# Kernel tuning notes

Measured on AMD Instinct MI355X. Metric: run time of the kernel, lower is better.

The kernel has to match this reference:

```python
import jax, jax.numpy as jnp
import numpy as np
from jax import lax

N, D_IN, D_H, D_A, N_CLS, K = 50000, 1024, 512, 256, 2, 8


def setup_inputs() -> dict:
    key = jax.random.key(0)
    ks = jax.random.split(key, 13)
    s = 0.02
    return {
        "h": jax.random.normal(ks[0], (1, N, D_IN), dtype=jnp.float32),
        "fc_W": jax.random.normal(ks[1], (D_H, D_IN), dtype=jnp.float32) * s,
        "fc_b": jnp.zeros((D_H,), jnp.float32),
        "att_a_W": jax.random.normal(ks[2], (D_A, D_H), dtype=jnp.float32) * s,
        "att_a_b": jnp.zeros((D_A,), jnp.float32),
        "att_b_W": jax.random.normal(ks[3], (D_A, D_H), dtype=jnp.float32) * s,
        "att_b_b": jnp.zeros((D_A,), jnp.float32),
        "att_c_W": jax.random.normal(ks[4], (1, D_A), dtype=jnp.float32) * s,
        "att_c_b": jnp.zeros((1,), jnp.float32),
        "cls_W": jax.random.normal(ks[5], (N_CLS, D_H), dtype=jnp.float32) * s,
        "cls_b": jnp.zeros((N_CLS,), jnp.float32),
        "inst_W": jax.random.normal(ks[6], (2, D_H), dtype=jnp.float32) * s,
        "inst_b": jnp.zeros((2,), jnp.float32),
        "label": 1,  # one_hot -> [0,1]: inst_eval runs only for classifier index 1
    }


def reference(h, fc_W, fc_b, att_a_W, att_a_b, att_b_W, att_b_b,
              att_c_W, att_c_b, cls_W, cls_b, inst_W, inst_b, label):
    x = jnp.squeeze(h, 0)                               # [N, 1024]
    hh = jax.nn.relu(x @ fc_W.T + fc_b)                 # [N, 512]
    # gated attention: tanh gate * sigmoid gate -> scalar score per instance
    a = jnp.tanh(hh @ att_a_W.T + att_a_b)              # [N, 256]
    b = jax.nn.sigmoid(hh @ att_b_W.T + att_b_b)        # [N, 256]
    A_raw = (a * b) @ att_c_W.T + att_c_b               # [N, 1]
    A = jax.nn.softmax(A_raw, axis=0)                   # softmax over instances

    # instance eval (label==1, subtyping=False -> only classifier index 1)
    scores = A_raw[:, 0]                                # [N]
    _, top_p_ids = lax.top_k(scores, K)
    _, top_n_ids = lax.top_k(-scores, K)
    ids = jnp.concatenate([top_p_ids, top_n_ids])       # [2K]
    inst = hh[ids]                                      # gather [2K, 512]
    logits = inst @ inst_W.T + inst_b                   # [2K, 2]
    targets = jnp.concatenate([jnp.ones((K,), jnp.int32),
                               jnp.zeros((K,), jnp.int32)])
    logp = jax.nn.log_softmax(logits, axis=-1)
    instance_loss = -jnp.mean(jnp.take_along_axis(logp, targets[:, None], axis=1))

    instance_scores = hh @ cls_W.T + cls_b              # [N, 2]
    preds = (instance_scores * A).sum(axis=0) / A.sum(axis=0)  # [2]
    preds = preds[None, :]                              # [1, 2]
    return preds, instance_scores, A_raw, instance_loss
```

## Files before the change

kernel.cpp:

```cpp
#include <hip/hip_runtime.h>
#include <hip/hip_bf16.h>
#include <math.h>

typedef __bf16 bf16_t;
typedef __bf16 bf16x8 __attribute__((ext_vector_type(8)));
typedef float  f32x4  __attribute__((ext_vector_type(4)));

#define NROWS 50000

typedef const __attribute__((address_space(1))) unsigned int* gp_t;
typedef __attribute__((address_space(3))) unsigned int* lp_t;
__device__ __forceinline__ void cp16(void* l, const void* g) {
    __builtin_amdgcn_global_load_lds((gp_t)g, (lp_t)l, 16, 0, 0);
}

__global__ void k_convert(const float* __restrict__ fcW,
                          const float* __restrict__ aW,
                          const float* __restrict__ bW,
                          bf16_t* __restrict__ permW1, bf16_t* __restrict__ permB2) {
    int t = blockIdx.x * 256 + threadIdx.x;
    {
        int row = t & 511, q = (t >> 9) & 3, kt = t >> 11;
        const float* src = fcW + (long)row * 1024 + kt * 32 + q * 8;
        bf16_t o[8];
        #pragma unroll
        for (int i = 0; i < 8; i++) o[i] = (bf16_t)src[i];
        *(bf16x8*)(permW1 + (long)t * 8) = *(bf16x8*)o;
    }
    if (t < 32768) {
        int row = t & 511, q = (t >> 9) & 3, kt = t >> 11;
        int g = row >> 4, u = g >> 1, j = u * 16 + (row & 15);
        const float* src = ((g & 1) ? bW : aW) + (long)j * 512 + kt * 32 + q * 8;
        bf16_t o[8];
        #pragma unroll
        for (int i = 0; i < 8; i++) o[i] = (bf16_t)src[i];
        *(bf16x8*)(permB2 + (long)t * 8) = *(bf16x8*)o;
    }
}

__global__ __launch_bounds__(512, 4) void k_gemm1(
        const float* __restrict__ x, const bf16_t* __restrict__ permW1,
        const float* __restrict__ fcb, bf16_t* __restrict__ hh) {
    __shared__ __align__(16) char smem[75776];

    const int tid = threadIdx.x;
    const int w  = tid >> 6;
    const int l  = tid & 63;
    const int q  = l >> 4;
    const int li = l & 15;
    const long row0 = (long)blockIdx.x * 64;

    f32x4 acc[4][4];
    #pragma unroll
    for (int a = 0; a < 4; a++)
        #pragma unroll
        for (int b = 0; b < 4; b++) acc[a][b] = (f32x4)0.0f;

    const int rx = tid >> 3;
    const int kx = (tid & 7) * 4;
    const long xrow = row0 + rx;
    const bool xvalid = (xrow < NROWS);
    const float* xp = x + xrow * 1024 + kx;

    float4 xv = xvalid ? *(const float4*)xp : make_float4(0.f, 0.f, 0.f, 0.f);
    {
        union { bf16_t h[4]; unsigned long long u; } pk;
        pk.h[0] = (bf16_t)xv.x; pk.h[1] = (bf16_t)xv.y;
        pk.h[2] = (bf16_t)xv.z; pk.h[3] = (bf16_t)xv.w;
        *(unsigned long long*)(smem + 65536 + (rx * 40 + kx) * 2) = pk.u;
    }
    xv = xvalid ? *(const float4*)(xp + 32) : make_float4(0.f, 0.f, 0.f, 0.f);
    {
        const bf16_t* gw = permW1 + (long)tid * 8;
        char* dst = smem + tid * 16;
        #pragma unroll
        for (int j = 0; j < 4; j++) cp16(dst + j * 8192, gw + j * 4096);
    }
    __syncthreads();

    for (int kt = 0; kt < 32; kt++) {
        const int cur = kt & 1;
        const int nxt = cur ^ 1;
        if (kt < 31) {
            const bf16_t* gw = permW1 + ((long)(kt + 1) * 2048 + tid) * 8;
            char* dst = smem + nxt * 32768 + tid * 16;
            #pragma unroll
            for (int j = 0; j < 4; j++) cp16(dst + j * 8192, gw + j * 4096);
            union { bf16_t h[4]; unsigned long long u; } pk;
            pk.h[0] = (bf16_t)xv.x; pk.h[1] = (bf16_t)xv.y;
            pk.h[2] = (bf16_t)xv.z; pk.h[3] = (bf16_t)xv.w;
            *(unsigned long long*)(smem + 65536 + nxt * 5120 + (rx * 40 + kx) * 2) = pk.u;
            int kn = (kt < 30 ? kt + 2 : 31) * 32;
            xv = xvalid ? *(const float4*)(xp + kn) : make_float4(0.f, 0.f, 0.f, 0.f);
        }
        const bf16_t* bsb = (const bf16_t*)(smem + cur * 32768);
        const bf16_t* xsb = (const bf16_t*)(smem + 65536 + cur * 5120);
        bf16x8 bfr[4];
        #pragma unroll
        for (int tn = 0; tn < 4; tn++)
            bfr[tn] = *(const bf16x8*)(bsb + q * 4096 + (w * 64 + tn * 16 + li) * 8);
        #pragma unroll
        for (int tm = 0; tm < 4; tm++) {
            bf16x8 af = *(const bf16x8*)(xsb + (tm * 16 + li) * 40 + q * 8);
            #pragma unroll
            for (int tn = 0; tn < 4; tn++)
                acc[tm][tn] = __builtin_amdgcn_mfma_f32_16x16x32_bf16(af, bfr[tn], acc[tm][tn], 0, 0, 0);
        }
        __syncthreads();
    }

    bf16_t* t16 = (bf16_t*)smem;
    float bias[4];
    #pragma unroll
    for (int tn = 0; tn < 4; tn++) bias[tn] = fcb[w * 64 + tn * 16 + li];

    const int rr = tid >> 5;
    const int cc = tid & 31;
    #pragma unroll
    for (int tm = 0; tm < 4; tm++) {
        #pragma unroll
        for (int tn = 0; tn < 4; tn++) {
            int col = w * 64 + tn * 16 + li;
            #pragma unroll
            for (int r = 0; r < 4; r++) {
                float v = acc[tm][tn][r] + bias[tn];
                v = v > 0.f ? v : 0.f;
                t16[(q * 4 + r) * 520 + col] = (bf16_t)v;
            }
        }
        __syncthreads();
        long row = row0 + tm * 16 + rr;
        if (row < NROWS) {
            bf16x8 v0 = *(const bf16x8*)&t16[rr * 520 + cc * 16];
            bf16x8 v1 = *(const bf16x8*)&t16[rr * 520 + cc * 16 + 8];
            *(bf16x8*)&hh[row * 512 + cc * 16] = v0;
            *(bf16x8*)&hh[row * 512 + cc * 16 + 8] = v1;
        }
        __syncthreads();
    }
}

__global__ __launch_bounds__(512, 4) void k_gemm2(
        const bf16_t* __restrict__ hh, const bf16_t* __restrict__ permB2,
        const float* __restrict__ aab, const float* __restrict__ abb,
        const float* __restrict__ acW, const float* __restrict__ acb,
        const float* __restrict__ clsW, const float* __restrict__ clsb,
        float* __restrict__ Araw, float* __restrict__ inst) {
    __shared__ __align__(16) char smem[73728];
    __shared__ bf16_t cls_lds[1024];

    const int tid = threadIdx.x;
    const int w  = tid >> 6;
    const int l  = tid & 63;
    const int q  = l >> 4;
    const int li = l & 15;
    const long row0 = (long)blockIdx.x * 64;

    if (tid < 128) {
        int c = tid >> 6, k8 = (tid & 63) * 8;
        #pragma unroll
        for (int i = 0; i < 8; i++)
            cls_lds[c * 512 + k8 + i] = (bf16_t)clsW[c * 512 + k8 + i];
    }

    f32x4 acc[4][4];
    #pragma unroll
    for (int a = 0; a < 4; a++)
        #pragma unroll
        for (int b = 0; b < 4; b++) acc[a][b] = (f32x4)0.0f;
    float cls0[4] = {0.f,0.f,0.f,0.f}, cls1[4] = {0.f,0.f,0.f,0.f};

    {
        const bf16_t* gb = permB2 + (long)tid * 8;
        char* dst = smem + 8192 + tid * 16;
        #pragma unroll
        for (int j = 0; j < 4; j++) cp16(dst + j * 8192, gb + j * 4096);
        if (tid < 256) {
            const bf16_t* ga = hh + (row0 + (tid >> 2)) * 512 + (tid & 3) * 8;
            cp16(smem + tid * 16, ga);
        }
    }
    __syncthreads();

    for (int kt = 0; kt < 16; kt++) {
        const int cur = kt & 1;
        const int nxt = cur ^ 1;
        if (kt < 15) {
            const bf16_t* gb = permB2 + ((long)(kt + 1) * 2048 + tid) * 8;
            char* dst = smem + 8192 + nxt * 32768 + tid * 16;
            #pragma unroll
            for (int j = 0; j < 4; j++) cp16(dst + j * 8192, gb + j * 4096);
            if (tid < 256) {
                const bf16_t* ga = hh + (row0 + (tid >> 2)) * 512 + (kt + 1) * 32 + (tid & 3) * 8;
                cp16(smem + nxt * 4096 + tid * 16, ga);
            }
        }
        const bf16_t* asb = (const bf16_t*)(smem + cur * 4096);
        const bf16_t* bsb = (const bf16_t*)(smem + 8192 + cur * 32768);
        bf16x8 bfr[4];
        #pragma unroll
        for (int tn = 0; tn < 4; tn++)
            bfr[tn] = *(const bf16x8*)(bsb + q * 4096 + (w * 64 + tn * 16 + li) * 8);
        const bool mycls = ((kt >> 1) == w);
        bf16x8 w0, w1;
        if (mycls) {
            w0 = *(const bf16x8*)&cls_lds[kt * 32 + q * 8];
            w1 = *(const bf16x8*)&cls_lds[512 + kt * 32 + q * 8];
        }
        #pragma unroll
        for (int tm = 0; tm < 4; tm++) {
            bf16x8 af = *(const bf16x8*)(asb + (tm * 16 + li) * 32 + q * 8);
            #pragma unroll
            for (int tn = 0; tn < 4; tn++)
                acc[tm][tn] = __builtin_amdgcn_mfma_f32_16x16x32_bf16(af, bfr[tn], acc[tm][tn], 0, 0, 0);
            if (mycls) {
                float s0 = 0.f, s1 = 0.f;
                #pragma unroll
                for (int jj = 0; jj < 8; jj++) {
                    float a = (float)af[jj];
                    s0 += a * (float)w0[jj];
                    s1 += a * (float)w1[jj];
                }
                cls0[tm] += s0; cls1[tm] += s1;
            }
        }
        __syncthreads();
    }

    float (*apart)[9] = (float (*)[9])smem;
    float (*cls_part)[64][2] = (float (*)[64][2])(smem + 4096);

    float sum_mr[4][4];
    #pragma unroll
    for (int a = 0; a < 4; a++)
        #pragma unroll
        for (int b = 0; b < 4; b++) sum_mr[a][b] = 0.f;
    #pragma unroll
    for (int p = 0; p < 2; p++) {
        int j = (w * 2 + p) * 16 + li;
        float ab_ = aab[j], bb_ = abb[j], cw = acW[j];
        int tn_a = p * 2, tn_b = p * 2 + 1;
        #pragma unroll
        for (int tm = 0; tm < 4; tm++)
            #pragma unroll
            for (int r = 0; r < 4; r++) {
                float av = tanhf(acc[tm][tn_a][r] + ab_);
                float bv = acc[tm][tn_b][r] + bb_;
                bv = 1.f / (1.f + expf(-bv));
                sum_mr[tm][r] += av * bv * cw;
            }
    }
    #pragma unroll
    for (int tm = 0; tm < 4; tm++)
        #pragma unroll
        for (int r = 0; r < 4; r++) {
            float v = sum_mr[tm][r];
            v += __shfl_xor(v, 1); v += __shfl_xor(v, 2);
            v += __shfl_xor(v, 4); v += __shfl_xor(v, 8);
            if (li == 0) apart[tm * 16 + q * 4 + r][w] = v;
        }
    #pragma unroll
    for (int tm = 0; tm < 4; tm++) {
        cls0[tm] += __shfl_xor(cls0[tm], 16); cls0[tm] += __shfl_xor(cls0[tm], 32);
        cls1[tm] += __shfl_xor(cls1[tm], 16); cls1[tm] += __shfl_xor(cls1[tm], 32);
        if (q == 0) {
            cls_part[w][tm * 16 + li][0] = cls0[tm];
            cls_part[w][tm * 16 + li][1] = cls1[tm];
        }
    }
    __syncthreads();
    if (tid < 64) {
        float s = acb[0];
        #pragma unroll
        for (int ww = 0; ww < 8; ww++) s += apart[tid][ww];
        long row = row0 + tid;
        if (row < NROWS) Araw[row] = s;
    }
    if (tid < 128) {
        int rr = tid >> 1, c = tid & 1;
        float s = clsb[c];
        #pragma unroll
        for (int ww = 0; ww < 8; ww++) s += cls_part[ww][rr][c];
        long row = row0 + rr;
        if (row < NROWS) inst[row * 2 + c] = s;
    }
}

__global__ void k_topk(const float* __restrict__ scores, int* __restrict__ ids,
                       float* __restrict__ sums) {
    __shared__ float cv[4096];
    __shared__ int   ci[4096];
    __shared__ float bwv[8]; __shared__ int bwi[8]; __shared__ int bws[8];
    int tid = threadIdx.x;
    int pass = blockIdx.x;
    if (pass == 0 && tid == 0) { sums[0] = 0.f; sums[1] = 0.f; sums[2] = 0.f; }
    float sign = (pass == 0) ? 1.f : -1.f;
    float tv[8]; int ti[8];
    #pragma unroll
    for (int k = 0; k < 8; k++) { tv[k] = -1e30f; ti[k] = 0x7fffffff; }
    for (int i = tid; i < NROWS; i += 512) {
        float v = sign * scores[i];
        if (v > tv[7] || (v == tv[7] && i < ti[7])) {
            int k = 7;
            while (k > 0 && (v > tv[k-1] || (v == tv[k-1] && i < ti[k-1]))) {
                tv[k] = tv[k-1]; ti[k] = ti[k-1]; k--;
            }
            tv[k] = v; ti[k] = i;
        }
    }
    for (int k = 0; k < 8; k++) { cv[tid * 8 + k] = tv[k]; ci[tid * 8 + k] = ti[k]; }
    __syncthreads();
    for (int r = 0; r < 8; r++) {
        float bv = -1e30f; int bi = 0x7fffffff, bslot = 0;
        for (int j = 0; j < 8; j++) {
            int s = tid + 512 * j;
            float v = cv[s]; int idx = ci[s];
            if (v > bv || (v == bv && idx < bi)) { bv = v; bi = idx; bslot = s; }
        }
        for (int m = 1; m < 64; m <<= 1) {
            float ov = __shfl_xor(bv, m); int oi = __shfl_xor(bi, m); int os = __shfl_xor(bslot, m);
            if (ov > bv || (ov == bv && oi < bi)) { bv = ov; bi = oi; bslot = os; }
        }
        if ((tid & 63) == 0) { bwv[tid >> 6] = bv; bwi[tid >> 6] = bi; bws[tid >> 6] = bslot; }
        __syncthreads();
        if (tid == 0) {
            float BV = -1e30f; int BI = 0x7fffffff, BS = 0;
            for (int wv = 0; wv < 8; wv++) {
                if (bwv[wv] > BV || (bwv[wv] == BV && bwi[wv] < BI)) { BV = bwv[wv]; BI = bwi[wv]; BS = bws[wv]; }
            }
            ids[pass * 8 + r] = BI;
            cv[BS] = -1e30f; ci[BS] = 0x7fffffff;
        }
        __syncthreads();
    }
}

__global__ void k_sum(const float* __restrict__ Araw, const float* __restrict__ inst,
                      const int* __restrict__ ids, float* sums) {
    __shared__ float r0[4], r1[4], r2[4];
    int tid = threadIdx.x;
    float mx = Araw[ids[0]];
    float se = 0.f, s0 = 0.f, s1 = 0.f;
    for (int i = blockIdx.x * 256 + tid; i < NROWS; i += 32768) {
        float e = expf(Araw[i] - mx);
        se += e; s0 += inst[2 * i] * e; s1 += inst[2 * i + 1] * e;
    }
    for (int s = 1; s < 64; s <<= 1) {
        se += __shfl_xor(se, s); s0 += __shfl_xor(s0, s); s1 += __shfl_xor(s1, s);
    }
    if ((tid & 63) == 0) { r0[tid >> 6] = se; r1[tid >> 6] = s0; r2[tid >> 6] = s1; }
    __syncthreads();
    if (tid == 0) {
        atomicAdd(&sums[0], r0[0] + r0[1] + r0[2] + r0[3]);
        atomicAdd(&sums[1], r1[0] + r1[1] + r1[2] + r1[3]);
        atomicAdd(&sums[2], r2[0] + r2[1] + r2[2] + r2[3]);
    }
}

__global__ void k_fin(const bf16_t* __restrict__ hh, const int* __restrict__ ids,
                      const float* __restrict__ sums, const float* __restrict__ instW,
                      const float* __restrict__ instb, float* __restrict__ dout) {
    __shared__ float lg[16][2];
    int tid = threadIdx.x;
    int r  = tid >> 4;
    int li = tid & 15;
    int id = ids[r];
    const bf16_t* hp = hh + (long)id * 512;
    float p0 = 0.f, p1 = 0.f;
    for (int k = li * 32; k < li * 32 + 32; k++) {
        float h = (float)hp[k];
        p0 += h * instW[k]; p1 += h * instW[512 + k];
    }
    for (int m = 1; m < 16; m <<= 1) { p0 += __shfl_xor(p0, m); p1 += __shfl_xor(p1, m); }
    if (li == 0) { lg[r][0] = p0 + instb[0]; lg[r][1] = p1 + instb[1]; }
    __syncthreads();
    if (tid == 0) {
        float loss = 0.f;
        for (int r2 = 0; r2 < 16; r2++) {
            float l0 = lg[r2][0], l1 = lg[r2][1];
            float mx = fmaxf(l0, l1);
            float lse = mx + logf(expf(l0 - mx) + expf(l1 - mx));
            float lt = (r2 < 8) ? l1 : l0;
            loss += (lse - lt);
        }
        dout[150002] = loss / 16.f;
        float se = sums[0];
        dout[0] = sums[1] / se;
        dout[1] = sums[2] / se;
    }
}

extern "C" void kernel_launch(void* const* d_in, const int* in_sizes, int n_in,
                              void* d_out, int out_size, void* d_ws, size_t ws_size,
                              hipStream_t stream) {
    const float* h   = (const float*)d_in[0];
    const float* fcW = (const float*)d_in[1];
    const float* fcb = (const float*)d_in[2];
    const float* aaW = (const float*)d_in[3];
    const float* aab = (const float*)d_in[4];
    const float* abW = (const float*)d_in[5];
    const float* abb = (const float*)d_in[6];
    const float* acW = (const float*)d_in[7];
    const float* acb = (const float*)d_in[8];
    const float* clW = (const float*)d_in[9];
    const float* clb = (const float*)d_in[10];
    const float* inW = (const float*)d_in[11];
    const float* inb = (const float*)d_in[12];
    float* out = (float*)d_out;

    char* ws = (char*)d_ws;
    bf16_t* hh      = (bf16_t*)(ws);
    bf16_t* permW1  = (bf16_t*)(ws + 51200000);
    bf16_t* permB2  = (bf16_t*)(ws + 52248576);
    float*  sums    = (float*) (ws + 52772864);
    int*    ids     = (int*)   (ws + 52772928);

    float* inst = out + 2;
    float* Araw = out + 2 + 100000;

    k_convert<<<256, 256, 0, stream>>>(fcW, aaW, abW, permW1, permB2);
    k_gemm1<<<782, 512, 0, stream>>>(h, permW1, fcb, hh);
    k_gemm2<<<782, 512, 0, stream>>>(hh, permB2, aab, abb, acW, acb, clW, clb, Araw, inst);
    k_topk<<<2, 512, 0, stream>>>(Araw, ids, sums);
    k_sum<<<128, 256, 0, stream>>>(Araw, inst, ids, sums);
    k_fin<<<1, 256, 0, stream>>>(hh, ids, sums, inW, inb, out);
}
```

Baseline: 547.7 us.

## Retile GEMM1 to 128x128 blocks, coalesce weight convert, split top-k across blocks

GEMM1 now uses 256-thread blocks computing 128x128 output tiles with a 2x2 wave layout and a swizzled block-to-tile mapping, so each X tile is reused by four column tiles that run close together in time, and LDS use per block drops. The weight conversion kernel now reads fp32 weights with coalesced float4 loads and scatters bf16 values into the permuted layout. Top-k is split across 8 blocks that each produce candidates, and the final selection merges them in k_fin, replacing the 2-block serial scan. Each row block of X is now read four times from global memory (by the four column-tile blocks), which relies on cache hits for efficiency.

```diff
diff --git a/kernel.cpp b/kernel.cpp
--- a/kernel.cpp
+++ b/kernel.cpp
@@ -3,6 +3,7 @@
 #include <math.h>
 
 typedef __bf16 bf16_t;
+typedef __bf16 bf16x4 __attribute__((ext_vector_type(4)));
 typedef __bf16 bf16x8 __attribute__((ext_vector_type(8)));
 typedef float  f32x4  __attribute__((ext_vector_type(4)));
 
@@ -19,122 +20,135 @@
                           const float* __restrict__ bW,
                           bf16_t* __restrict__ permW1, bf16_t* __restrict__ permB2) {
     int t = blockIdx.x * 256 + threadIdx.x;
-    {
-        int row = t & 511, q = (t >> 9) & 3, kt = t >> 11;
-        const float* src = fcW + (long)row * 1024 + kt * 32 + q * 8;
-        bf16_t o[8];
-        #pragma unroll
-        for (int i = 0; i < 8; i++) o[i] = (bf16_t)src[i];
-        *(bf16x8*)(permW1 + (long)t * 8) = *(bf16x8*)o;
-    }
-    if (t < 32768) {
-        int row = t & 511, q = (t >> 9) & 3, kt = t >> 11;
-        int g = row >> 4, u = g >> 1, j = u * 16 + (row & 15);
-        const float* src = ((g & 1) ? bW : aW) + (long)j * 512 + kt * 32 + q * 8;
-        bf16_t o[8];
-        #pragma unroll
-        for (int i = 0; i < 8; i++) o[i] = (bf16_t)src[i];
-        *(bf16x8*)(permB2 + (long)t * 8) = *(bf16x8*)o;
-    }
-}
-
-__global__ __launch_bounds__(512, 4) void k_gemm1(
+    if (t < 131072) {
+        float4 v = *(const float4*)(fcW + (long)t * 4);
+        int row = t >> 8;
+        int k0 = (t & 255) * 4;
+        int kt = k0 >> 5, q = (k0 >> 3) & 3, j = k0 & 7;
+        bf16_t o[4] = {(bf16_t)v.x, (bf16_t)v.y, (bf16_t)v.z, (bf16_t)v.w};
+        *(bf16x4*)(permW1 + kt * 16384 + q * 4096 + row * 8 + j) = *(bf16x4*)o;
+    } else {
+        int t2 = t - 131072;
+        int isB = t2 >> 15;
+        int f = t2 & 32767;
+        float4 v = *(const float4*)(((isB ? bW : aW)) + (long)f * 4);
+        int srow = f >> 7;
+        int k0 = (f & 127) * 4;
+        int kt = k0 >> 5, q = (k0 >> 3) & 3, j = k0 & 7;
+        int r = ((srow >> 4) * 2 + isB) * 16 + (srow & 15);
+        bf16_t o[4] = {(bf16_t)v.x, (bf16_t)v.y, (bf16_t)v.z, (bf16_t)v.w};
+        *(bf16x4*)(permB2 + kt * 16384 + q * 4096 + r * 8 + j) = *(bf16x4*)o;
+    }
+}
+
+__global__ __launch_bounds__(256, 4) void k_gemm1(
         const float* __restrict__ x, const bf16_t* __restrict__ permW1,
         const float* __restrict__ fcb, bf16_t* __restrict__ hh) {
-    __shared__ __align__(16) char smem[75776];
-
+    __shared__ __align__(16) char smem[32768];
     const int tid = threadIdx.x;
-    const int w  = tid >> 6;
-    const int l  = tid & 63;
-    const int q  = l >> 4;
-    const int li = l & 15;
-    const long row0 = (long)blockIdx.x * 64;
+    const int w = tid >> 6, l = tid & 63, q = l >> 4, li = l & 15;
+    const int wr = w >> 1, wc = w & 1;
+    const int b = blockIdx.x;
+    const int rtile = (b & 7) | ((b >> 5) << 3);
+    const int ctile = (b >> 3) & 3;
+    const long row0 = (long)rtile * 128;
+    const int col0 = ctile * 128;
 
     f32x4 acc[4][4];
     #pragma unroll
     for (int a = 0; a < 4; a++)
         #pragma unroll
-        for (int b = 0; b < 4; b++) acc[a][b] = (f32x4)0.0f;
-
-    const int rx = tid >> 3;
-    const int kx = (tid & 7) * 4;
-    const long xrow = row0 + rx;
-    const bool xvalid = (xrow < NROWS);
-    const float* xp = x + xrow * 1024 + kx;
-
-    float4 xv = xvalid ? *(const float4*)xp : make_float4(0.f, 0.f, 0.f, 0.f);
-    {
-        union { bf16_t h[4]; unsigned long long u; } pk;
-        pk.h[0] = (bf16_t)xv.x; pk.h[1] = (bf16_t)xv.y;
-        pk.h[2] = (bf16_t)xv.z; pk.h[3] = (bf16_t)xv.w;
-        *(unsigned long long*)(smem + 65536 + (rx * 40 + kx) * 2) = pk.u;
-    }
-    xv = xvalid ? *(const float4*)(xp + 32) : make_float4(0.f, 0.f, 0.f, 0.f);
-    {
-        const bf16_t* gw = permW1 + (long)tid * 8;
-        char* dst = smem + tid * 16;
-        #pragma unroll
-        for (int j = 0; j < 4; j++) cp16(dst + j * 8192, gw + j * 4096);
-    }
+        for (int c = 0; c < 4; c++) acc[a][c] = (f32x4)0.0f;
+
+    int arow[4], akx[4]; bool avalid[4];
+    #pragma unroll
+    for (int j = 0; j < 4; j++) {
+        int s = j * 256 + tid;
+        arow[j] = s >> 3; akx[j] = s & 7;
+        avalid[j] = (row0 + arow[j]) < NROWS;
+    }
+    const float* xbase = x + row0 * 1024;
+
+    float4 xv[4];
+    #pragma unroll
+    for (int j = 0; j < 4; j++)
+        xv[j] = avalid[j] ? *(const float4*)(xbase + arow[j] * 1024 + akx[j] * 4)
+                          : make_float4(0.f, 0.f, 0.f, 0.f);
+    #pragma unroll
+    for (int j = 0; j < 4; j++) {
+        bf16_t o[4] = {(bf16_t)xv[j].x, (bf16_t)xv[j].y, (bf16_t)xv[j].z, (bf16_t)xv[j].w};
+        *(bf16x4*)(smem + (akx[j] >> 1) * 2048 + arow[j] * 16 + (akx[j] & 1) * 8) = *(bf16x4*)o;
+    }
+    #pragma unroll
+    for (int s2 = 0; s2 < 2; s2++) {
+        int s = tid + s2 * 256;
+        cp16(smem + 16384 + s * 16, permW1 + (s >> 7) * 4096 + (col0 + (s & 127)) * 8);
+    }
+    #pragma unroll
+    for (int j = 0; j < 4; j++)
+        xv[j] = avalid[j] ? *(const float4*)(xbase + arow[j] * 1024 + 32 + akx[j] * 4)
+                          : make_float4(0.f, 0.f, 0.f, 0.f);
     __syncthreads();
 
     for (int kt = 0; kt < 32; kt++) {
-        const int cur = kt & 1;
-        const int nxt = cur ^ 1;
+        const int cur = kt & 1, nxt = cur ^ 1;
         if (kt < 31) {
-            const bf16_t* gw = permW1 + ((long)(kt + 1) * 2048 + tid) * 8;
-            char* dst = smem + nxt * 32768 + tid * 16;
-            #pragma unroll
-            for (int j = 0; j < 4; j++) cp16(dst + j * 8192, gw + j * 4096);
-            union { bf16_t h[4]; unsigned long long u; } pk;
-            pk.h[0] = (bf16_t)xv.x; pk.h[1] = (bf16_t)xv.y;
-            pk.h[2] = (bf16_t)xv.z; pk.h[3] = (bf16_t)xv.w;
-            *(unsigned long long*)(smem + 65536 + nxt * 5120 + (rx * 40 + kx) * 2) = pk.u;
+            const bf16_t* gsrc = permW1 + (long)(kt + 1) * 16384;
+            #pragma unroll
+            for (int s2 = 0; s2 < 2; s2++) {
+                int s = tid + s2 * 256;
+                cp16(smem + 16384 + nxt * 8192 + s * 16, gsrc + (s >> 7) * 4096 + (col0 + (s & 127)) * 8);
+            }
+            #pragma unroll
+            for (int j = 0; j < 4; j++) {
+                bf16_t o[4] = {(bf16_t)xv[j].x, (bf16_t)xv[j].y, (bf16_t)xv[j].z, (bf16_t)xv[j].w};
+                *(bf16x4*)(smem + nxt * 8192 + (akx[j] >> 1) * 2048 + arow[j] * 16 + (akx[j] & 1) * 8) = *(bf16x4*)o;
+            }
             int kn = (kt < 30 ? kt + 2 : 31) * 32;
-            xv = xvalid ? *(const float4*)(xp + kn) : make_float4(0.f, 0.f, 0.f, 0.f);
-        }
-        const bf16_t* bsb = (const bf16_t*)(smem + cur * 32768);
-        const bf16_t* xsb = (const bf16_t*)(smem + 65536 + cur * 5120);
-        bf16x8 bfr[4];
+            #pragma unroll
+            for (int j = 0; j < 4; j++)
+                xv[j] = avalid[j] ? *(const float4*)(xbase + arow[j] * 1024 + kn + akx[j] * 4)
+                                  : make_float4(0.f, 0.f, 0.f, 0.f);
+        }
+        const bf16_t* Ab = (const bf16_t*)(smem + cur * 8192);
+        const bf16_t* Bb = (const bf16_t*)(smem + 16384 + cur * 8192);
+        bf16x8 afr[4], bfr[4];
         #pragma unroll
         for (int tn = 0; tn < 4; tn++)
-            bfr[tn] = *(const bf16x8*)(bsb + q * 4096 + (w * 64 + tn * 16 + li) * 8);
-        #pragma unroll
-        for (int tm = 0; tm < 4; tm++) {
-            bf16x8 af = *(const bf16x8*)(xsb + (tm * 16 + li) * 40 + q * 8);
+            bfr[tn] = *(const bf16x8*)(Bb + q * 1024 + (wc * 64 + tn * 16 + li) * 8);
+        #pragma unroll
+        for (int tm = 0; tm < 4; tm++)
+            afr[tm] = *(const bf16x8*)(Ab + q * 1024 + (wr * 64 + tm * 16 + li) * 8);
+        #pragma unroll
+        for (int tm = 0; tm < 4; tm++)
             #pragma unroll
             for (int tn = 0; tn < 4; tn++)
-                acc[tm][tn] = __builtin_amdgcn_mfma_f32_16x16x32_bf16(af, bfr[tn], acc[tm][tn], 0, 0, 0);
-        }
+                acc[tm][tn] = __builtin_amdgcn_mfma_f32_16x16x32_bf16(afr[tm], bfr[tn], acc[tm][tn], 0, 0, 0);
         __syncthreads();
     }
 
     bf16_t* t16 = (bf16_t*)smem;
     float bias[4];
     #pragma unroll
-    for (int tn = 0; tn < 4; tn++) bias[tn] = fcb[w * 64 + tn * 16 + li];
-
-    const int rr = tid >> 5;
-    const int cc = tid & 31;
+    for (int tn = 0; tn < 4; tn++) bias[tn] = fcb[col0 + wc * 64 + tn * 16 + li];
+    const int rr = tid >> 3, cc = tid & 7;
     #pragma unroll
     for (int tm = 0; tm < 4; tm++) {
         #pragma unroll
-        for (int tn = 0; tn < 4; tn++) {
-            int col = w * 64 + tn * 16 + li;
+        for (int tn = 0; tn < 4; tn++)
             #pragma unroll
             for (int r = 0; r < 4; r++) {
                 float v = acc[tm][tn][r] + bias[tn];
                 v = v > 0.f ? v : 0.f;
-                t16[(q * 4 + r) * 520 + col] = (bf16_t)v;
-            }
-        }
-        __syncthreads();
-        long row = row0 + tm * 16 + rr;
-        if (row < NROWS) {
-            bf16x8 v0 = *(const bf16x8*)&t16[rr * 520 + cc * 16];
-            bf16x8 v1 = *(const bf16x8*)&t16[rr * 520 + cc * 16 + 8];
-            *(bf16x8*)&hh[row * 512 + cc * 16] = v0;
-            *(bf16x8*)&hh[row * 512 + cc * 16 + 8] = v1;
+                t16[(wr * 16 + q * 4 + r) * 136 + wc * 64 + tn * 16 + li] = (bf16_t)v;
+            }
+        __syncthreads();
+        long grow = row0 + ((rr >> 4) * 64) + tm * 16 + (rr & 15);
+        if (grow < NROWS) {
+            bf16x8 v0 = *(const bf16x8*)&t16[rr * 136 + cc * 16];
+            bf16x8 v1 = *(const bf16x8*)&t16[rr * 136 + cc * 16 + 8];
+            *(bf16x8*)&hh[grow * 512 + col0 + cc * 16] = v0;
+            *(bf16x8*)&hh[grow * 512 + col0 + cc * 16 + 8] = v1;
         }
         __syncthreads();
     }
@@ -146,14 +160,11 @@
         const float* __restrict__ acW, const float* __restrict__ acb,
         const float* __restrict__ clsW, const float* __restrict__ clsb,
         float* __restrict__ Araw, float* __restrict__ inst) {
-    __shared__ __align__(16) char smem[73728];
-    __shared__ bf16_t cls_lds[1024];
+    __shared__ __align__(16) char smem[75776];
+    bf16_t* cls_lds = (bf16_t*)(smem + 73728);
 
     const int tid = threadIdx.x;
-    const int w  = tid >> 6;
-    const int l  = tid & 63;
-    const int q  = l >> 4;
-    const int li = l & 15;
+    const int w = tid >> 6, l = tid & 63, q = l >> 4, li = l & 15;
     const long row0 = (long)blockIdx.x * 64;
 
     if (tid < 128) {
@@ -167,7 +178,7 @@
     #pragma unroll
     for (int a = 0; a < 4; a++)
         #pragma unroll
-        for (int b = 0; b < 4; b++) acc[a][b] = (f32x4)0.0f;
+        for (int c = 0; c < 4; c++) acc[a][c] = (f32x4)0.0f;
     float cls0[4] = {0.f,0.f,0.f,0.f}, cls1[4] = {0.f,0.f,0.f,0.f};
 
     {
@@ -183,8 +194,7 @@
     __syncthreads();
 
     for (int kt = 0; kt < 16; kt++) {
-        const int cur = kt & 1;
-        const int nxt = cur ^ 1;
+        const int cur = kt & 1, nxt = cur ^ 1;
         if (kt < 15) {
             const bf16_t* gb = permB2 + ((long)(kt + 1) * 2048 + tid) * 8;
             char* dst = smem + 8192 + nxt * 32768 + tid * 16;
@@ -234,7 +244,7 @@
     #pragma unroll
     for (int a = 0; a < 4; a++)
         #pragma unroll
-        for (int b = 0; b < 4; b++) sum_mr[a][b] = 0.f;
+        for (int c = 0; c < 4; c++) sum_mr[a][c] = 0.f;
     #pragma unroll
     for (int p = 0; p < 2; p++) {
         int j = (w * 2 + p) * 16 + li;
@@ -286,60 +296,68 @@
     }
 }
 
-__global__ void k_topk(const float* __restrict__ scores, int* __restrict__ ids,
-                       float* __restrict__ sums) {
+__global__ void k_topk_part(const float* __restrict__ scores,
+                            float* __restrict__ candV, int* __restrict__ candI,
+                            float* __restrict__ sums) {
     __shared__ float cv[4096];
     __shared__ int   ci[4096];
     __shared__ float bwv[8]; __shared__ int bwi[8]; __shared__ int bws[8];
     int tid = threadIdx.x;
-    int pass = blockIdx.x;
-    if (pass == 0 && tid == 0) { sums[0] = 0.f; sums[1] = 0.f; sums[2] = 0.f; }
-    float sign = (pass == 0) ? 1.f : -1.f;
-    float tv[8]; int ti[8];
-    #pragma unroll
-    for (int k = 0; k < 8; k++) { tv[k] = -1e30f; ti[k] = 0x7fffffff; }
-    for (int i = tid; i < NROWS; i += 512) {
-        float v = sign * scores[i];
-        if (v > tv[7] || (v == tv[7] && i < ti[7])) {
-            int k = 7;
-            while (k > 0 && (v > tv[k-1] || (v == tv[k-1] && i < ti[k-1]))) {
-                tv[k] = tv[k-1]; ti[k] = ti[k-1]; k--;
-            }
-            tv[k] = v; ti[k] = i;
-        }
-    }
-    for (int k = 0; k < 8; k++) { cv[tid * 8 + k] = tv[k]; ci[tid * 8 + k] = ti[k]; }
-    __syncthreads();
-    for (int r = 0; r < 8; r++) {
-        float bv = -1e30f; int bi = 0x7fffffff, bslot = 0;
-        for (int j = 0; j < 8; j++) {
-            int s = tid + 512 * j;
-            float v = cv[s]; int idx = ci[s];
-            if (v > bv || (v == bv && idx < bi)) { bv = v; bi = idx; bslot = s; }
-        }
-        for (int m = 1; m < 64; m <<= 1) {
-            float ov = __shfl_xor(bv, m); int oi = __shfl_xor(bi, m); int os = __shfl_xor(bslot, m);
-            if (ov > bv || (ov == bv && oi < bi)) { bv = ov; bi = oi; bslot = os; }
-        }
-        if ((tid & 63) == 0) { bwv[tid >> 6] = bv; bwi[tid >> 6] = bi; bws[tid >> 6] = bslot; }
-        __syncthreads();
-        if (tid == 0) {
-            float BV = -1e30f; int BI = 0x7fffffff, BS = 0;
-            for (int wv = 0; wv < 8; wv++) {
-                if (bwv[wv] > BV || (bwv[wv] == BV && bwi[wv] < BI)) { BV = bwv[wv]; BI = bwi[wv]; BS = bws[wv]; }
-            }
-            ids[pass * 8 + r] = BI;
-            cv[BS] = -1e30f; ci[BS] = 0x7fffffff;
+    int p = blockIdx.x;
+    if (p == 0 && tid == 0) { sums[0] = 0.f; sums[1] = 0.f; sums[2] = 0.f; }
+    int lo = p * 6250, hi = lo + 6250;
+    for (int pass = 0; pass < 2; pass++) {
+        float sign = (pass == 0) ? 1.f : -1.f;
+        float tv[8]; int ti[8];
+        #pragma unroll
+        for (int k = 0; k < 8; k++) { tv[k] = -1e30f; ti[k] = 0x7fffffff; }
+        for (int i = lo + tid; i < hi; i += 512) {
+            float v = sign * scores[i];
+            if (v > tv[7] || (v == tv[7] && i < ti[7])) {
+                int k = 7;
+                while (k > 0 && (v > tv[k-1] || (v == tv[k-1] && i < ti[k-1]))) {
+                    tv[k] = tv[k-1]; ti[k] = ti[k-1]; k--;
+                }
+                tv[k] = v; ti[k] = i;
+            }
+        }
+        for (int k = 0; k < 8; k++) { cv[tid * 8 + k] = tv[k]; ci[tid * 8 + k] = ti[k]; }
+        __syncthreads();
+        for (int r = 0; r < 8; r++) {
+            float bv = -1e30f; int bi = 0x7fffffff, bslot = 0;
+            for (int j = 0; j < 8; j++) {
+                int s = tid + 512 * j;
+                float v = cv[s]; int idx = ci[s];
+                if (v > bv || (v == bv && idx < bi)) { bv = v; bi = idx; bslot = s; }
+            }
+            for (int m = 1; m < 64; m <<= 1) {
+                float ov = __shfl_xor(bv, m); int oi = __shfl_xor(bi, m); int os = __shfl_xor(bslot, m);
+                if (ov > bv || (ov == bv && oi < bi)) { bv = ov; bi = oi; bslot = os; }
+            }
+            if ((tid & 63) == 0) { bwv[tid >> 6] = bv; bwi[tid >> 6] = bi; bws[tid >> 6] = bslot; }
+            __syncthreads();
+            if (tid == 0) {
+                float BV = -1e30f; int BI = 0x7fffffff, BS = 0;
+                for (int wv = 0; wv < 8; wv++) {
+                    if (bwv[wv] > BV || (bwv[wv] == BV && bwi[wv] < BI)) { BV = bwv[wv]; BI = bwi[wv]; BS = bws[wv]; }
+                }
+                candV[pass * 64 + p * 8 + r] = BV;
+                candI[pass * 64 + p * 8 + r] = BI;
+                cv[BS] = -1e30f; ci[BS] = 0x7fffffff;
+            }
+            __syncthreads();
         }
         __syncthreads();
     }
 }
 
 __global__ void k_sum(const float* __restrict__ Araw, const float* __restrict__ inst,
-                      const int* __restrict__ ids, float* sums) {
+                      const float* __restrict__ candV, float* sums) {
     __shared__ float r0[4], r1[4], r2[4];
     int tid = threadIdx.x;
-    float mx = Araw[ids[0]];
+    float mx = -1e30f;
+    #pragma unroll
+    for (int p = 0; p < 8; p++) mx = fmaxf(mx, candV[p * 8]);
     float se = 0.f, s0 = 0.f, s1 = 0.f;
     for (int i = blockIdx.x * 256 + tid; i < NROWS; i += 32768) {
         float e = expf(Araw[i] - mx);
@@ -357,14 +375,30 @@
     }
 }
 
-__global__ void k_fin(const bf16_t* __restrict__ hh, const int* __restrict__ ids,
+__global__ void k_fin(const bf16_t* __restrict__ hh,
+                      const float* __restrict__ candV, const int* __restrict__ candI,
                       const float* __restrict__ sums, const float* __restrict__ instW,
                       const float* __restrict__ instb, float* __restrict__ dout) {
+    __shared__ int mid[16];
     __shared__ float lg[16][2];
     int tid = threadIdx.x;
-    int r  = tid >> 4;
-    int li = tid & 15;
-    int id = ids[r];
+    int wv = tid >> 6, l = tid & 63;
+    if (wv < 2) {
+        float v = candV[wv * 64 + l];
+        int idx = candI[wv * 64 + l];
+        for (int r = 0; r < 8; r++) {
+            float bv = v; int bi = idx; int bs = l;
+            for (int m = 1; m < 64; m <<= 1) {
+                float ov = __shfl_xor(bv, m); int oi = __shfl_xor(bi, m); int os = __shfl_xor(bs, m);
+                if (ov > bv || (ov == bv && oi < bi)) { bv = ov; bi = oi; bs = os; }
+            }
+            if (l == 0) mid[wv * 8 + r] = bi;
+            if (l == bs) v = -1e30f;
+        }
+    }
+    __syncthreads();
+    int r = tid >> 4, li = tid & 15;
+    int id = mid[r];
     const bf16_t* hp = hh + (long)id * 512;
     float p0 = 0.f, p1 = 0.f;
     for (int k = li * 32; k < li * 32 + 32; k++) {
@@ -412,16 +446,17 @@
     bf16_t* hh      = (bf16_t*)(ws);
     bf16_t* permW1  = (bf16_t*)(ws + 51200000);
     bf16_t* permB2  = (bf16_t*)(ws + 52248576);
-    float*  sums    = (float*) (ws + 52772864);
-    int*    ids     = (int*)   (ws + 52772928);
+    float*  candV   = (float*) (ws + 52772864);
+    int*    candI   = (int*)   (ws + 52773888);
+    float*  sums    = (float*) (ws + 52774912);
 
     float* inst = out + 2;
     float* Araw = out + 2 + 100000;
 
-    k_convert<<<256, 256, 0, stream>>>(fcW, aaW, abW, permW1, permB2);
-    k_gemm1<<<782, 512, 0, stream>>>(h, permW1, fcb, hh);
+    k_convert<<<768, 256, 0, stream>>>(fcW, aaW, abW, permW1, permB2);
+    k_gemm1<<<1568, 256, 0, stream>>>(h, permW1, fcb, hh);
     k_gemm2<<<782, 512, 0, stream>>>(hh, permB2, aab, abb, acW, acb, clW, clb, Araw, inst);
-    k_topk<<<2, 512, 0, stream>>>(Araw, ids, sums);
-    k_sum<<<128, 256, 0, stream>>>(Araw, inst, ids, sums);
-    k_fin<<<1, 256, 0, stream>>>(hh, ids, sums, inW, inb, out);
-}
+    k_topk_part<<<8, 512, 0, stream>>>(Araw, candV, candI, sums);
+    k_sum<<<128, 256, 0, stream>>>(Araw, inst, candV, sums);
+    k_fin<<<1, 256, 0, stream>>>(hh, candV, candI, sums, inW, inb, out);
+}
```

After: 488.1 us. 10.9% less time.
